# Performance work log

Hardware: AMD Instinct MI355X
Metric: run time of the kernel (lower is better)

## Reference

```python
import jax, jax.numpy as jnp
import numpy as np
from math import sqrt

W_SIZE = jnp.array([32, 64, 128, 256, 32, 64, 128, 256], dtype=jnp.int32)  # per-head window

def setup_inputs() -> dict:
    key = jax.random.key(0)
    kq, kk, kv = jax.random.split(key, 3)
    B, L, H, E = 4, 2048, 8, 64
    D = 64
    return {
        "queries": jax.random.normal(kq, (B, L, H, E), dtype=jnp.float32),
        "keys": jax.random.normal(kk, (B, L, H, E), dtype=jnp.float32),
        "values": jax.random.normal(kv, (B, L, H, D), dtype=jnp.float32),
    }

def reference(queries, keys, values):
    B, L, H, E = queries.shape
    scale = 1.0 / sqrt(E)
    # dense scores: [B, H, L, L]
    scores = jnp.einsum('blhe,bshe->bhls', queries, keys)
    # per-head band mask: |i - j| <= w[h]  -> [H, L, L]
    i = jnp.arange(L)
    diff = jnp.abs(i[:, None] - i[None, :])            # [L, L]
    band = diff[None, :, :] <= W_SIZE[:, None, None]   # [H, L, L]
    scores = jnp.where(band[None], scores, -jnp.inf)
    A = jax.nn.softmax(scale * scores, axis=-1)        # dropout p=0 (eval)
    V = jnp.einsum('bhls,bshd->blhd', A, values)
    return V
```

## Files before the change

kernel.cpp:

```cpp
#include <hip/hip_runtime.h>
#include <math.h>


#define LL 2048
#define HH 8
#define EE 64
#define DD 64
#define RS (HH * EE)

typedef __attribute__((ext_vector_type(8))) short short8;
typedef __attribute__((ext_vector_type(4))) float floatx4;
typedef __attribute__((ext_vector_type(4))) _Float16 half4;
typedef __attribute__((ext_vector_type(2))) __fp16 fp16x2;

static __device__ __forceinline__ unsigned f2bf(float f) {
    union { float f; unsigned u; } v; v.f = f;
    return (v.u + 0x7fff + ((v.u >> 16) & 1)) >> 16;
}
static __device__ __forceinline__ unsigned pack2(float a, float b) {
    return f2bf(a) | (f2bf(b) << 16);
}
static __device__ __forceinline__ unsigned packh2(float a, float b) {
    union { fp16x2 h; unsigned u; } v;
    v.h = __builtin_amdgcn_cvt_pkrtz(a, b);
    return v.u;
}

__global__ __launch_bounds__(256, 4) void mwa_r7(
    const float* __restrict__ Q,
    const float* __restrict__ K,
    const float* __restrict__ V,
    float* __restrict__ O)
{
    const int tid  = threadIdx.x;
    const int lane = tid & 63;
    const int wv   = tid >> 6;
    const int quad = lane >> 4;
    const int l15  = lane & 15;

    const int gid = blockIdx.x;
    const int kb  = gid >> 8;
    const int c   = gid & 255;
    const int b   = kb;
    const int it  = c >> 3;
    const int h   = (((c >> 2) & 1) << 2) | ((kb + c) & 3);
    const int i0  = it << 6;
    const int w   = 32 << (h & 3);

    alignas(16) __shared__ short sK [2][4096];
    alignas(16) __shared__ short sVt[2][64 * 72];

    const float* Qb = Q + ((size_t)b * LL * HH + h) * EE;
    const float* Kb = K + ((size_t)b * LL * HH + h) * EE;
    const float* Vb = V + ((size_t)b * LL * HH + h) * DD;
    float*       Ob = O + ((size_t)b * LL * HH + h) * DD;

    {
        const float sc = 0.125f;
        const int row = tid >> 2, cc = (tid & 3) << 4;
        const float4* src = (const float4*)(Qb + (size_t)(i0 + row) * RS + cc);
        float4 f0 = src[0], f1 = src[1], f2 = src[2], f3 = src[3];
        uint4 u0 = { pack2(sc*f0.x,sc*f0.y), pack2(sc*f0.z,sc*f0.w),
                     pack2(sc*f1.x,sc*f1.y), pack2(sc*f1.z,sc*f1.w) };
        uint4 u1 = { pack2(sc*f2.x,sc*f2.y), pack2(sc*f2.z,sc*f2.w),
                     pack2(sc*f3.x,sc*f3.y), pack2(sc*f3.z,sc*f3.w) };
        uint4* dst = (uint4*)&sK[0][row * 72 + cc];
        dst[0] = u0; dst[1] = u1;
    }
    __syncthreads();
    short8 qf0, qf1;
    {
        const short* p = &sK[0][(wv * 16 + l15) * 72 + quad * 8];
        qf0 = *(const short8*)p;
        qf1 = *(const short8*)(p + 32);
    }
    __syncthreads();

    const int jt_lo = max(0, i0 - w) >> 6;
    const int jt_hi = min(LL - 1, i0 + 63 + w) >> 6;

    {
        const int j0 = jt_lo << 6;
        const int row = tid >> 2, cc = (tid & 3) << 4;
        const float4* src = (const float4*)(Kb + (size_t)(j0 + row) * RS + cc);
        float4 f0 = src[0], f1 = src[1], f2 = src[2], f3 = src[3];
        float vv[16];
#pragma unroll
        for (int rr = 0; rr < 16; ++rr)
            vv[rr] = Vb[(size_t)(j0 + wv * 16 + rr) * RS + lane];

        uint4 u0 = { pack2(f0.x,f0.y), pack2(f0.z,f0.w), pack2(f1.x,f1.y), pack2(f1.z,f1.w) };
        uint4 u1 = { pack2(f2.x,f2.y), pack2(f2.z,f2.w), pack2(f3.x,f3.y), pack2(f3.z,f3.w) };
        const int jtw = row >> 4, l15w = row & 15, ks = cc >> 5, q0 = (cc >> 3) & 3;
        *(uint4*)&sK[0][(((jtw * 2 + ks) * 4 + q0    ) * 16 + l15w) * 8] = u0;
        *(uint4*)&sK[0][(((jtw * 2 + ks) * 4 + q0 + 1) * 16 + l15w) * 8] = u1;

        uint4 w0 = { packh2(vv[0],vv[1]),  packh2(vv[2],vv[3]),
                     packh2(vv[4],vv[5]),  packh2(vv[6],vv[7]) };
        uint4 w1 = { packh2(vv[8],vv[9]),  packh2(vv[10],vv[11]),
                     packh2(vv[12],vv[13]), packh2(vv[14],vv[15]) };
        *(uint4*)&sVt[0][lane * 72 + wv * 16    ] = w0;
        *(uint4*)&sVt[0][lane * 72 + wv * 16 + 8] = w1;
    }
    __syncthreads();

    floatx4 acc[4] = {};
    float lsum = 0.f;
    const int iq = i0 + wv * 16 + l15;

    for (int jt = jt_lo; jt <= jt_hi; ++jt) {
        const int cur = (jt - jt_lo) & 1;
        const int nxt = cur ^ 1;
        const bool more = jt < jt_hi;
        const int j0 = jt << 6;

        float4 kf0, kf1, kf2, kf3;
        float vv[16];
        const int rowp = tid >> 2, cp = (tid & 3) << 4;
        if (more) {
            const int jn = (jt + 1) << 6;
            const float4* src = (const float4*)(Kb + (size_t)(jn + rowp) * RS + cp);
            kf0 = src[0]; kf1 = src[1]; kf2 = src[2]; kf3 = src[3];
#pragma unroll
            for (int rr = 0; rr < 16; ++rr)
                vv[rr] = Vb[(size_t)(jn + wv * 16 + rr) * RS + lane];
        }

        const bool full = ((i0 + 63 - j0) <= w) && ((j0 + 63 - i0) <= w);
        half4 pf[4];
#pragma unroll
        for (int t4 = 0; t4 < 4; ++t4) {
            const short* kp = &sK[cur][1024 * t4 + 128 * quad + 8 * l15];
            short8 k0 = *(const short8*)kp;
            short8 k1 = *(const short8*)(kp + 512);
            floatx4 st = {};
            st = __builtin_amdgcn_mfma_f32_16x16x32_bf16(k0, qf0, st, 0, 0, 0);
            st = __builtin_amdgcn_mfma_f32_16x16x32_bf16(k1, qf1, st, 0, 0, 0);

            float p[4];
            const int jb = j0 + t4 * 16 + quad * 4;
#pragma unroll
            for (int r = 0; r < 4; ++r) {
                float x = st[r];
                if (!full) {
                    const int di = iq - (jb + r);
                    x = (di <= w && di >= -w) ? x : -INFINITY;
                }
                p[r] = __expf(x);
                lsum += p[r];
            }
            union { half4 v; unsigned u[2]; } pu;
            pu.u[0] = packh2(p[0], p[1]);
            pu.u[1] = packh2(p[2], p[3]);
            pf[t4] = pu.v;
        }

#pragma unroll
        for (int nt = 0; nt < 4; ++nt) {
            const short* vbase = &sVt[cur][(nt * 16 + l15) * 72];
#pragma unroll
            for (int t4 = 0; t4 < 4; ++t4) {
                half4 vf = *(const half4*)(vbase + t4 * 16 + quad * 4);
                acc[nt] = __builtin_amdgcn_mfma_f32_16x16x16f16(pf[t4], vf, acc[nt], 0, 0, 0);
            }
        }

        if (more) {
            uint4 u0 = { pack2(kf0.x,kf0.y), pack2(kf0.z,kf0.w), pack2(kf1.x,kf1.y), pack2(kf1.z,kf1.w) };
            uint4 u1 = { pack2(kf2.x,kf2.y), pack2(kf2.z,kf2.w), pack2(kf3.x,kf3.y), pack2(kf3.z,kf3.w) };
            const int jtw = rowp >> 4, l15w = rowp & 15, ks = cp >> 5, q0 = (cp >> 3) & 3;
            *(uint4*)&sK[nxt][(((jtw * 2 + ks) * 4 + q0    ) * 16 + l15w) * 8] = u0;
            *(uint4*)&sK[nxt][(((jtw * 2 + ks) * 4 + q0 + 1) * 16 + l15w) * 8] = u1;

            uint4 w0 = { packh2(vv[0],vv[1]),  packh2(vv[2],vv[3]),
                         packh2(vv[4],vv[5]),  packh2(vv[6],vv[7]) };
            uint4 w1 = { packh2(vv[8],vv[9]),  packh2(vv[10],vv[11]),
                         packh2(vv[12],vv[13]), packh2(vv[14],vv[15]) };
            *(uint4*)&sVt[nxt][lane * 72 + wv * 16    ] = w0;
            *(uint4*)&sVt[nxt][lane * 72 + wv * 16 + 8] = w1;
        }
        __syncthreads();
    }

    lsum += __shfl_xor(lsum, 16, 64);
    lsum += __shfl_xor(lsum, 32, 64);
    float rinv[4];
#pragma unroll
    for (int r = 0; r < 4; ++r) {
        const float lr = __shfl(lsum, quad * 4 + r, 64);
        rinv[r] = 1.0f / lr;
    }
#pragma unroll
    for (int nt = 0; nt < 4; ++nt) {
#pragma unroll
        for (int r = 0; r < 4; ++r) {
            Ob[(size_t)(i0 + wv * 16 + quad * 4 + r) * RS + nt * 16 + l15]
                = acc[nt][r] * rinv[r];
        }
    }
}

extern "C" void kernel_launch(void* const* d_in, const int* in_sizes, int n_in,
                              void* d_out, int out_size, void* d_ws, size_t ws_size,
                              hipStream_t stream)
{
    const float* Q = (const float*)d_in[0];
    const float* K = (const float*)d_in[1];
    const float* V = (const float*)d_in[2];
    float* O = (float*)d_out;

    dim3 grid(4 * HH * (LL / 64)), block(256);
    hipLaunchKernelGGL(mwa_r7, grid, block, 0, stream, Q, K, V, O);
}
```

Before: 104.5 us.

## Split key tiles across two wave groups per block and merge partial sums

Doubles the block to 512 threads so two groups of four waves each process alternating key/value tiles for the same 64-query tile. Each group keeps its own double-buffered LDS, and at the end group 1 writes its partial accumulators and row sums through LDS for group 0 to add before normalising and storing. The block index mapping is also changed so the widest-window heads are scheduled first, which should reduce tail imbalance. The aim is to shorten the per-block serial loop over key tiles. The cost is double the LDS per block, lower achievable occupancy, and an extra merge step.

```diff
diff --git a/kernel.cpp b/kernel.cpp
--- a/kernel.cpp
+++ b/kernel.cpp
@@ -26,7 +26,7 @@
     return v.u;
 }
 
-__global__ __launch_bounds__(256, 4) void mwa_r7(
+__global__ __launch_bounds__(512, 4) void mwa_r8(
     const float* __restrict__ Q,
     const float* __restrict__ K,
     const float* __restrict__ V,
@@ -34,21 +34,24 @@
 {
     const int tid  = threadIdx.x;
     const int lane = tid & 63;
-    const int wv   = tid >> 6;
+    const int grp  = tid >> 8;
+    const int tid8 = tid & 255;
+    const int wv   = (tid >> 6) & 3;
     const int quad = lane >> 4;
     const int l15  = lane & 15;
 
     const int gid = blockIdx.x;
-    const int kb  = gid >> 8;
-    const int c   = gid & 255;
-    const int b   = kb;
-    const int it  = c >> 3;
-    const int h   = (((c >> 2) & 1) << 2) | ((kb + c) & 3);
+    const int k   = gid >> 8;
+    const int r   = gid & 255;
+    const int it  = r >> 3;
+    const int b   = (r >> 1) & 3;
+    const int hb  = r & 1;
+    const int h   = hb * 4 + (3 - k);
     const int i0  = it << 6;
-    const int w   = 32 << (h & 3);
-
-    alignas(16) __shared__ short sK [2][4096];
-    alignas(16) __shared__ short sVt[2][64 * 72];
+    const int w   = 32 << (3 - k);
+
+    alignas(16) __shared__ short sK [2][2][4096];
+    alignas(16) __shared__ short sVt[2][2][64 * 72];
 
     const float* Qb = Q + ((size_t)b * LL * HH + h) * EE;
     const float* Kb = K + ((size_t)b * LL * HH + h) * EE;
@@ -57,20 +60,17 @@
 
     {
         const float sc = 0.125f;
-        const int row = tid >> 2, cc = (tid & 3) << 4;
+        const int row = tid >> 3, cc = (tid & 7) << 3;
         const float4* src = (const float4*)(Qb + (size_t)(i0 + row) * RS + cc);
-        float4 f0 = src[0], f1 = src[1], f2 = src[2], f3 = src[3];
+        float4 f0 = src[0], f1 = src[1];
         uint4 u0 = { pack2(sc*f0.x,sc*f0.y), pack2(sc*f0.z,sc*f0.w),
                      pack2(sc*f1.x,sc*f1.y), pack2(sc*f1.z,sc*f1.w) };
-        uint4 u1 = { pack2(sc*f2.x,sc*f2.y), pack2(sc*f2.z,sc*f2.w),
-                     pack2(sc*f3.x,sc*f3.y), pack2(sc*f3.z,sc*f3.w) };
-        uint4* dst = (uint4*)&sK[0][row * 72 + cc];
-        dst[0] = u0; dst[1] = u1;
+        *(uint4*)&(((short*)sK)[row * 72 + cc]) = u0;
     }
     __syncthreads();
     short8 qf0, qf1;
     {
-        const short* p = &sK[0][(wv * 16 + l15) * 72 + quad * 8];
+        const short* p = &(((short*)sK)[(wv * 16 + l15) * 72 + quad * 8]);
         qf0 = *(const short8*)p;
         qf1 = *(const short8*)(p + 32);
     }
@@ -78,10 +78,13 @@
 
     const int jt_lo = max(0, i0 - w) >> 6;
     const int jt_hi = min(LL - 1, i0 + 63 + w) >> 6;
+    const int n     = jt_hi - jt_lo + 1;
+    const int ng    = (n - grp + 1) >> 1;
+    const int nIter = (n + 1) >> 1;
 
     {
-        const int j0 = jt_lo << 6;
-        const int row = tid >> 2, cc = (tid & 3) << 4;
+        const int j0 = (jt_lo + grp) << 6;
+        const int row = tid8 >> 2, cc = (tid8 & 3) << 4;
         const float4* src = (const float4*)(Kb + (size_t)(j0 + row) * RS + cc);
         float4 f0 = src[0], f1 = src[1], f2 = src[2], f3 = src[3];
         float vv[16];
@@ -92,15 +95,15 @@
         uint4 u0 = { pack2(f0.x,f0.y), pack2(f0.z,f0.w), pack2(f1.x,f1.y), pack2(f1.z,f1.w) };
         uint4 u1 = { pack2(f2.x,f2.y), pack2(f2.z,f2.w), pack2(f3.x,f3.y), pack2(f3.z,f3.w) };
         const int jtw = row >> 4, l15w = row & 15, ks = cc >> 5, q0 = (cc >> 3) & 3;
-        *(uint4*)&sK[0][(((jtw * 2 + ks) * 4 + q0    ) * 16 + l15w) * 8] = u0;
-        *(uint4*)&sK[0][(((jtw * 2 + ks) * 4 + q0 + 1) * 16 + l15w) * 8] = u1;
+        *(uint4*)&sK[grp][0][(((jtw * 2 + ks) * 4 + q0    ) * 16 + l15w) * 8] = u0;
+        *(uint4*)&sK[grp][0][(((jtw * 2 + ks) * 4 + q0 + 1) * 16 + l15w) * 8] = u1;
 
         uint4 w0 = { packh2(vv[0],vv[1]),  packh2(vv[2],vv[3]),
                      packh2(vv[4],vv[5]),  packh2(vv[6],vv[7]) };
         uint4 w1 = { packh2(vv[8],vv[9]),  packh2(vv[10],vv[11]),
                      packh2(vv[12],vv[13]), packh2(vv[14],vv[15]) };
-        *(uint4*)&sVt[0][lane * 72 + wv * 16    ] = w0;
-        *(uint4*)&sVt[0][lane * 72 + wv * 16 + 8] = w1;
+        *(uint4*)&sVt[grp][0][lane * 72 + wv * 16    ] = w0;
+        *(uint4*)&sVt[grp][0][lane * 72 + wv * 16 + 8] = w1;
     }
     __syncthreads();
 
@@ -108,17 +111,19 @@
     float lsum = 0.f;
     const int iq = i0 + wv * 16 + l15;
 
-    for (int jt = jt_lo; jt <= jt_hi; ++jt) {
-        const int cur = (jt - jt_lo) & 1;
+    for (int s = 0; s < nIter; ++s) {
+        const int cur = s & 1;
         const int nxt = cur ^ 1;
-        const bool more = jt < jt_hi;
+        const bool act  = s < ng;
+        const bool more = (s + 1) < ng;
+        const int jt = jt_lo + grp + 2 * s;
         const int j0 = jt << 6;
 
         float4 kf0, kf1, kf2, kf3;
         float vv[16];
-        const int rowp = tid >> 2, cp = (tid & 3) << 4;
+        const int rowp = tid8 >> 2, cp = (tid8 & 3) << 4;
         if (more) {
-            const int jn = (jt + 1) << 6;
+            const int jn = (jt + 2) << 6;
             const float4* src = (const float4*)(Kb + (size_t)(jn + rowp) * RS + cp);
             kf0 = src[0]; kf1 = src[1]; kf2 = src[2]; kf3 = src[3];
 #pragma unroll
@@ -126,42 +131,44 @@
                 vv[rr] = Vb[(size_t)(jn + wv * 16 + rr) * RS + lane];
         }
 
-        const bool full = ((i0 + 63 - j0) <= w) && ((j0 + 63 - i0) <= w);
-        half4 pf[4];
-#pragma unroll
-        for (int t4 = 0; t4 < 4; ++t4) {
-            const short* kp = &sK[cur][1024 * t4 + 128 * quad + 8 * l15];
-            short8 k0 = *(const short8*)kp;
-            short8 k1 = *(const short8*)(kp + 512);
-            floatx4 st = {};
-            st = __builtin_amdgcn_mfma_f32_16x16x32_bf16(k0, qf0, st, 0, 0, 0);
-            st = __builtin_amdgcn_mfma_f32_16x16x32_bf16(k1, qf1, st, 0, 0, 0);
-
-            float p[4];
-            const int jb = j0 + t4 * 16 + quad * 4;
-#pragma unroll
-            for (int r = 0; r < 4; ++r) {
-                float x = st[r];
-                if (!full) {
-                    const int di = iq - (jb + r);
-                    x = (di <= w && di >= -w) ? x : -INFINITY;
+        if (act) {
+            const bool full = ((i0 + 63 - j0) <= w) && ((j0 + 63 - i0) <= w);
+            half4 pf[4];
+#pragma unroll
+            for (int t4 = 0; t4 < 4; ++t4) {
+                const short* kp = &sK[grp][cur][1024 * t4 + 128 * quad + 8 * l15];
+                short8 k0 = *(const short8*)kp;
+                short8 k1 = *(const short8*)(kp + 512);
+                floatx4 st = {};
+                st = __builtin_amdgcn_mfma_f32_16x16x32_bf16(k0, qf0, st, 0, 0, 0);
+                st = __builtin_amdgcn_mfma_f32_16x16x32_bf16(k1, qf1, st, 0, 0, 0);
+
+                float p[4];
+                const int jb = j0 + t4 * 16 + quad * 4;
+#pragma unroll
+                for (int rr2 = 0; rr2 < 4; ++rr2) {
+                    float x = st[rr2];
+                    if (!full) {
+                        const int di = iq - (jb + rr2);
+                        x = (di <= w && di >= -w) ? x : -INFINITY;
+                    }
+                    p[rr2] = __expf(x);
+                    lsum += p[rr2];
                 }
-                p[r] = __expf(x);
-                lsum += p[r];
+                union { half4 v; unsigned u[2]; } pu;
+                pu.u[0] = packh2(p[0], p[1]);
+                pu.u[1] = packh2(p[2], p[3]);
+                pf[t4] = pu.v;
             }
-            union { half4 v; unsigned u[2]; } pu;
-            pu.u[0] = packh2(p[0], p[1]);
-            pu.u[1] = packh2(p[2], p[3]);
-            pf[t4] = pu.v;
-        }
-
-#pragma unroll
-        for (int nt = 0; nt < 4; ++nt) {
-            const short* vbase = &sVt[cur][(nt * 16 + l15) * 72];
-#pragma unroll
-            for (int t4 = 0; t4 < 4; ++t4) {
-                half4 vf = *(const half4*)(vbase + t4 * 16 + quad * 4);
-                acc[nt] = __builtin_amdgcn_mfma_f32_16x16x16f16(pf[t4], vf, acc[nt], 0, 0, 0);
+
+#pragma unroll
+            for (int nt = 0; nt < 4; ++nt) {
+                const short* vbase = &sVt[grp][cur][(nt * 16 + l15) * 72];
+#pragma unroll
+                for (int t4 = 0; t4 < 4; ++t4) {
+                    half4 vf = *(const half4*)(vbase + t4 * 16 + quad * 4);
+                    acc[nt] = __builtin_amdgcn_mfma_f32_16x16x16f16(pf[t4], vf, acc[nt], 0, 0, 0);
+                }
             }
         }
 
@@ -169,33 +176,54 @@
             uint4 u0 = { pack2(kf0.x,kf0.y), pack2(kf0.z,kf0.w), pack2(kf1.x,kf1.y), pack2(kf1.z,kf1.w) };
             uint4 u1 = { pack2(kf2.x,kf2.y), pack2(kf2.z,kf2.w), pack2(kf3.x,kf3.y), pack2(kf3.z,kf3.w) };
             const int jtw = rowp >> 4, l15w = rowp & 15, ks = cp >> 5, q0 = (cp >> 3) & 3;
-            *(uint4*)&sK[nxt][(((jtw * 2 + ks) * 4 + q0    ) * 16 + l15w) * 8] = u0;
-            *(uint4*)&sK[nxt][(((jtw * 2 + ks) * 4 + q0 + 1) * 16 + l15w) * 8] = u1;
+            *(uint4*)&sK[grp][nxt][(((jtw * 2 + ks) * 4 + q0    ) * 16 + l15w) * 8] = u0;
+            *(uint4*)&sK[grp][nxt][(((jtw * 2 + ks) * 4 + q0 + 1) * 16 + l15w) * 8] = u1;
 
             uint4 w0 = { packh2(vv[0],vv[1]),  packh2(vv[2],vv[3]),
                          packh2(vv[4],vv[5]),  packh2(vv[6],vv[7]) };
             uint4 w1 = { packh2(vv[8],vv[9]),  packh2(vv[10],vv[11]),
                          packh2(vv[12],vv[13]), packh2(vv[14],vv[15]) };
-            *(uint4*)&sVt[nxt][lane * 72 + wv * 16    ] = w0;
-            *(uint4*)&sVt[nxt][lane * 72 + wv * 16 + 8] = w1;
+            *(uint4*)&sVt[grp][nxt][lane * 72 + wv * 16    ] = w0;
+            *(uint4*)&sVt[grp][nxt][lane * 72 + wv * 16 + 8] = w1;
         }
         __syncthreads();
     }
 
     lsum += __shfl_xor(lsum, 16, 64);
     lsum += __shfl_xor(lsum, 32, 64);
-    float rinv[4];
-#pragma unroll
-    for (int r = 0; r < 4; ++r) {
-        const float lr = __shfl(lsum, quad * 4 + r, 64);
-        rinv[r] = 1.0f / lr;
-    }
-#pragma unroll
-    for (int nt = 0; nt < 4; ++nt) {
-#pragma unroll
-        for (int r = 0; r < 4; ++r) {
-            Ob[(size_t)(i0 + wv * 16 + quad * 4 + r) * RS + nt * 16 + l15]
-                = acc[nt][r] * rinv[r];
+
+    float* mrg = (float*)&sK[0][0][0];
+    float* lsA = (float*)&sVt[0][0][0];
+
+    if (grp == 1) {
+#pragma unroll
+        for (int nt = 0; nt < 4; ++nt)
+            *(floatx4*)&mrg[(tid8 * 4 + nt) * 4] = acc[nt];
+        if (quad == 0) lsA[wv * 16 + l15] = lsum;
+    }
+    __syncthreads();
+
+    if (grp == 0) {
+        lsum += lsA[wv * 16 + l15];
+#pragma unroll
+        for (int nt = 0; nt < 4; ++nt) {
+            floatx4 o = *(const floatx4*)&mrg[(tid8 * 4 + nt) * 4];
+            acc[nt][0] += o[0]; acc[nt][1] += o[1];
+            acc[nt][2] += o[2]; acc[nt][3] += o[3];
+        }
+        float rinv[4];
+#pragma unroll
+        for (int rr2 = 0; rr2 < 4; ++rr2) {
+            const float lr = __shfl(lsum, quad * 4 + rr2, 64);
+            rinv[rr2] = 1.0f / lr;
+        }
+#pragma unroll
+        for (int nt = 0; nt < 4; ++nt) {
+#pragma unroll
+            for (int rr2 = 0; rr2 < 4; ++rr2) {
+                Ob[(size_t)(i0 + wv * 16 + quad * 4 + rr2) * RS + nt * 16 + l15]
+                    = acc[nt][rr2] * rinv[rr2];
+            }
         }
     }
 }
@@ -209,6 +237,6 @@
     const float* V = (const float*)d_in[2];
     float* O = (float*)d_out;
 
-    dim3 grid(4 * HH * (LL / 64)), block(256);
-    hipLaunchKernelGGL(mwa_r7, grid, block, 0, stream, Q, K, V, O);
-}
+    dim3 grid(4 * HH * (LL / 64)), block(512);
+    hipLaunchKernelGGL(mwa_r8, grid, block, 0, stream, Q, K, V, O);
+}
```

New measurement: 104.0 us. No clear change (-0.5%).

## Double query tile to 128 rows with 8 waves sharing K/V tiles

Applied to the files above, without the earlier changes.

Each block now handles 128 query rows with 512 threads (8 waves) instead of 64 rows with 256 threads. Every staged 64-row K/V tile is reused by twice as many queries, roughly halving global K/V traffic and conversion work per query. The grid is reordered so blocks for heavy (wide-window) heads are dispatched before light ones, which is meant to balance load. In exchange there are fewer, larger blocks (512) and more register and LDS pressure per block. The band also covers a taller query tile, so more masked-out columns are computed near tile edges.

```diff
diff --git a/kernel.cpp b/kernel.cpp
--- a/kernel.cpp
+++ b/kernel.cpp
@@ -26,7 +26,10 @@
     return v.u;
 }
 
-__global__ __launch_bounds__(256, 4) void mwa_r7(
+#define K_BUF(cu)  (sAll + (cu) * 4096)
+#define V_BUF(cu)  (sAll + 8192 + (cu) * 4608)
+
+__global__ __launch_bounds__(512, 4) void mwa_r9(
     const float* __restrict__ Q,
     const float* __restrict__ K,
     const float* __restrict__ V,
@@ -38,17 +41,20 @@
     const int quad = lane >> 4;
     const int l15  = lane & 15;
 
-    const int gid = blockIdx.x;
-    const int kb  = gid >> 8;
-    const int c   = gid & 255;
-    const int b   = kb;
-    const int it  = c >> 3;
-    const int h   = (((c >> 2) & 1) << 2) | ((kb + c) & 3);
-    const int i0  = it << 6;
-    const int w   = 32 << (h & 3);
-
-    alignas(16) __shared__ short sK [2][4096];
-    alignas(16) __shared__ short sVt[2][64 * 72];
+    const int gid   = blockIdx.x;
+    const int heavy = (gid >> 8) == 0;
+    const int c     = gid & 255;
+    const int it    = c >> 4;
+    const int rem   = c & 15;
+    const int b     = rem >> 2;
+    const int z     = rem & 3;
+    const int hb    = z >> 1;
+    const int p     = z & 1;
+    const int h     = hb * 4 + (heavy ? (3 - p) : p);
+    const int i0    = it << 7;
+    const int w     = 32 << (h & 3);
+
+    alignas(16) __shared__ short sAll[17408];
 
     const float* Qb = Q + ((size_t)b * LL * HH + h) * EE;
     const float* Kb = K + ((size_t)b * LL * HH + h) * EE;
@@ -64,43 +70,38 @@
                      pack2(sc*f1.x,sc*f1.y), pack2(sc*f1.z,sc*f1.w) };
         uint4 u1 = { pack2(sc*f2.x,sc*f2.y), pack2(sc*f2.z,sc*f2.w),
                      pack2(sc*f3.x,sc*f3.y), pack2(sc*f3.z,sc*f3.w) };
-        uint4* dst = (uint4*)&sK[0][row * 72 + cc];
+        uint4* dst = (uint4*)&sAll[row * 72 + cc];
         dst[0] = u0; dst[1] = u1;
     }
     __syncthreads();
     short8 qf0, qf1;
     {
-        const short* p = &sK[0][(wv * 16 + l15) * 72 + quad * 8];
-        qf0 = *(const short8*)p;
-        qf1 = *(const short8*)(p + 32);
+        const short* qp = &sAll[(wv * 16 + l15) * 72 + quad * 8];
+        qf0 = *(const short8*)qp;
+        qf1 = *(const short8*)(qp + 32);
     }
     __syncthreads();
 
     const int jt_lo = max(0, i0 - w) >> 6;
-    const int jt_hi = min(LL - 1, i0 + 63 + w) >> 6;
+    const int jt_hi = min(LL - 1, i0 + 127 + w) >> 6;
 
     {
         const int j0 = jt_lo << 6;
-        const int row = tid >> 2, cc = (tid & 3) << 4;
+        const int row = tid >> 3, cc = (tid & 7) << 3;
         const float4* src = (const float4*)(Kb + (size_t)(j0 + row) * RS + cc);
-        float4 f0 = src[0], f1 = src[1], f2 = src[2], f3 = src[3];
-        float vv[16];
-#pragma unroll
-        for (int rr = 0; rr < 16; ++rr)
-            vv[rr] = Vb[(size_t)(j0 + wv * 16 + rr) * RS + lane];
+        float4 f0 = src[0], f1 = src[1];
+        float vv[8];
+#pragma unroll
+        for (int rr = 0; rr < 8; ++rr)
+            vv[rr] = Vb[(size_t)(j0 + wv * 8 + rr) * RS + lane];
 
         uint4 u0 = { pack2(f0.x,f0.y), pack2(f0.z,f0.w), pack2(f1.x,f1.y), pack2(f1.z,f1.w) };
-        uint4 u1 = { pack2(f2.x,f2.y), pack2(f2.z,f2.w), pack2(f3.x,f3.y), pack2(f3.z,f3.w) };
         const int jtw = row >> 4, l15w = row & 15, ks = cc >> 5, q0 = (cc >> 3) & 3;
-        *(uint4*)&sK[0][(((jtw * 2 + ks) * 4 + q0    ) * 16 + l15w) * 8] = u0;
-        *(uint4*)&sK[0][(((jtw * 2 + ks) * 4 + q0 + 1) * 16 + l15w) * 8] = u1;
-
-        uint4 w0 = { packh2(vv[0],vv[1]),  packh2(vv[2],vv[3]),
-                     packh2(vv[4],vv[5]),  packh2(vv[6],vv[7]) };
-        uint4 w1 = { packh2(vv[8],vv[9]),  packh2(vv[10],vv[11]),
-                     packh2(vv[12],vv[13]), packh2(vv[14],vv[15]) };
-        *(uint4*)&sVt[0][lane * 72 + wv * 16    ] = w0;
-        *(uint4*)&sVt[0][lane * 72 + wv * 16 + 8] = w1;
+        *(uint4*)&K_BUF(0)[(((jtw * 2 + ks) * 4 + q0) * 16 + l15w) * 8] = u0;
+
+        uint4 w0 = { packh2(vv[0],vv[1]), packh2(vv[2],vv[3]),
+                     packh2(vv[4],vv[5]), packh2(vv[6],vv[7]) };
+        *(uint4*)&V_BUF(0)[lane * 72 + wv * 8] = w0;
     }
     __syncthreads();
 
@@ -114,30 +115,30 @@
         const bool more = jt < jt_hi;
         const int j0 = jt << 6;
 
-        float4 kf0, kf1, kf2, kf3;
-        float vv[16];
-        const int rowp = tid >> 2, cp = (tid & 3) << 4;
+        float4 kf0, kf1;
+        float vv[8];
+        const int rowp = tid >> 3, cp = (tid & 7) << 3;
         if (more) {
             const int jn = (jt + 1) << 6;
             const float4* src = (const float4*)(Kb + (size_t)(jn + rowp) * RS + cp);
-            kf0 = src[0]; kf1 = src[1]; kf2 = src[2]; kf3 = src[3];
-#pragma unroll
-            for (int rr = 0; rr < 16; ++rr)
-                vv[rr] = Vb[(size_t)(jn + wv * 16 + rr) * RS + lane];
-        }
-
-        const bool full = ((i0 + 63 - j0) <= w) && ((j0 + 63 - i0) <= w);
+            kf0 = src[0]; kf1 = src[1];
+#pragma unroll
+            for (int rr = 0; rr < 8; ++rr)
+                vv[rr] = Vb[(size_t)(jn + wv * 8 + rr) * RS + lane];
+        }
+
+        const bool full = ((i0 + 127 - j0) <= w) && ((j0 + 63 - i0) <= w);
         half4 pf[4];
 #pragma unroll
         for (int t4 = 0; t4 < 4; ++t4) {
-            const short* kp = &sK[cur][1024 * t4 + 128 * quad + 8 * l15];
+            const short* kp = &K_BUF(cur)[1024 * t4 + 128 * quad + 8 * l15];
             short8 k0 = *(const short8*)kp;
             short8 k1 = *(const short8*)(kp + 512);
             floatx4 st = {};
             st = __builtin_amdgcn_mfma_f32_16x16x32_bf16(k0, qf0, st, 0, 0, 0);
             st = __builtin_amdgcn_mfma_f32_16x16x32_bf16(k1, qf1, st, 0, 0, 0);
 
-            float p[4];
+            float pr[4];
             const int jb = j0 + t4 * 16 + quad * 4;
 #pragma unroll
             for (int r = 0; r < 4; ++r) {
@@ -146,18 +147,18 @@
                     const int di = iq - (jb + r);
                     x = (di <= w && di >= -w) ? x : -INFINITY;
                 }
-                p[r] = __expf(x);
-                lsum += p[r];
+                pr[r] = __expf(x);
+                lsum += pr[r];
             }
             union { half4 v; unsigned u[2]; } pu;
-            pu.u[0] = packh2(p[0], p[1]);
-            pu.u[1] = packh2(p[2], p[3]);
+            pu.u[0] = packh2(pr[0], pr[1]);
+            pu.u[1] = packh2(pr[2], pr[3]);
             pf[t4] = pu.v;
         }
 
 #pragma unroll
         for (int nt = 0; nt < 4; ++nt) {
-            const short* vbase = &sVt[cur][(nt * 16 + l15) * 72];
+            const short* vbase = &V_BUF(cur)[(nt * 16 + l15) * 72];
 #pragma unroll
             for (int t4 = 0; t4 < 4; ++t4) {
                 half4 vf = *(const half4*)(vbase + t4 * 16 + quad * 4);
@@ -166,18 +167,14 @@
         }
 
         if (more) {
-            uint4 u0 = { pack2(kf0.x,kf0.y), pack2(kf0.z,kf0.w), pack2(kf1.x,kf1.y), pack2(kf1.z,kf1.w) };
-            uint4 u1 = { pack2(kf2.x,kf2.y), pack2(kf2.z,kf2.w), pack2(kf3.x,kf3.y), pack2(kf3.z,kf3.w) };
+            uint4 u0 = { pack2(kf0.x,kf0.y), pack2(kf0.z,kf0.w),
+                         pack2(kf1.x,kf1.y), pack2(kf1.z,kf1.w) };
             const int jtw = rowp >> 4, l15w = rowp & 15, ks = cp >> 5, q0 = (cp >> 3) & 3;
-            *(uint4*)&sK[nxt][(((jtw * 2 + ks) * 4 + q0    ) * 16 + l15w) * 8] = u0;
-            *(uint4*)&sK[nxt][(((jtw * 2 + ks) * 4 + q0 + 1) * 16 + l15w) * 8] = u1;
-
-            uint4 w0 = { packh2(vv[0],vv[1]),  packh2(vv[2],vv[3]),
-                         packh2(vv[4],vv[5]),  packh2(vv[6],vv[7]) };
-            uint4 w1 = { packh2(vv[8],vv[9]),  packh2(vv[10],vv[11]),
-                         packh2(vv[12],vv[13]), packh2(vv[14],vv[15]) };
-            *(uint4*)&sVt[nxt][lane * 72 + wv * 16    ] = w0;
-            *(uint4*)&sVt[nxt][lane * 72 + wv * 16 + 8] = w1;
+            *(uint4*)&K_BUF(nxt)[(((jtw * 2 + ks) * 4 + q0) * 16 + l15w) * 8] = u0;
+
+            uint4 w0 = { packh2(vv[0],vv[1]), packh2(vv[2],vv[3]),
+                         packh2(vv[4],vv[5]), packh2(vv[6],vv[7]) };
+            *(uint4*)&V_BUF(nxt)[lane * 72 + wv * 8] = w0;
         }
         __syncthreads();
     }
@@ -209,6 +206,6 @@
     const float* V = (const float*)d_in[2];
     float* O = (float*)d_out;
 
-    dim3 grid(4 * HH * (LL / 64)), block(256);
-    hipLaunchKernelGGL(mwa_r7, grid, block, 0, stream, Q, K, V, O);
-}
+    dim3 grid(512), block(512);
+    hipLaunchKernelGGL(mwa_r9, grid, block, 0, stream, Q, K, V, O);
+}
```

Result: faster. 101.6 us (-2.7%).
